# Kernel optimization log

Measured on AMD Instinct MI355X. Metric: run time of the kernel, lower is better.

The kernel has to match this reference:

```python
import jax, jax.numpy as jnp
import numpy as np

N = 4_194_304      # number of coordinate samples
H = 4              # hidden_features
L = 256            # hidden_layers
FIRST_OMEGA = 3000.0
HIDDEN_OMEGA = 30.0


def setup_inputs() -> dict:
    key = jax.random.key(0)
    ks = jax.random.split(key, 11)
    coords = jax.random.normal(ks[0], (N, 1), dtype=jnp.float32)
    # first layer: weight uniform(-1/in_features, 1/in_features), in_features=1
    w_first = jax.random.uniform(ks[1], (H, 1), jnp.float32, -1.0, 1.0)
    b_first = jax.random.uniform(ks[2], (H,), jnp.float32, -1.0, 1.0)
    # hidden layers: uniform(-sqrt(6/H)/omega, +)
    c_hid = float(np.sqrt(6.0 / H) / HIDDEN_OMEGA)
    w_hidden = jax.random.uniform(ks[3], (L, H, H), jnp.float32, -c_hid, c_hid)
    b_hidden = jax.random.uniform(ks[4], (L, H), jnp.float32, -c_hid, c_hid)
    # outermost linear, same init const
    w_out = jax.random.uniform(ks[5], (1, H), jnp.float32, -c_hid, c_hid)
    b_out = jax.random.uniform(ks[6], (1,), jnp.float32, -c_hid, c_hid)
    # harmonizer scalars (a,b,c,d); near 0 so exp(a)~1
    a_param = (jax.random.normal(ks[7], (), jnp.float32) * 0.1)
    b_param = (jax.random.normal(ks[8], (), jnp.float32) * 0.1)
    c_param = (jax.random.normal(ks[9], (), jnp.float32) * 0.1)
    d_param = (jax.random.normal(ks[10], (), jnp.float32) * 0.1)
    return {
        "coords": coords,
        "w_first": w_first, "b_first": b_first,
        "w_hidden": w_hidden, "b_hidden": b_hidden,
        "w_out": w_out, "b_out": b_out,
        "a_param": a_param, "b_param": b_param,
        "c_param": c_param, "d_param": d_param,
    }


def reference(coords, w_first, b_first, w_hidden, b_hidden, w_out, b_out,
              a_param, b_param, c_param, d_param):
    amp = jnp.exp(a_param)
    freq = jnp.exp(b_param)
    # first sine layer, omega_0 = 3000
    x = amp * jnp.sin(freq * FIRST_OMEGA * (coords @ w_first.T + b_first) + c_param) + d_param
    # 256 hidden sine layers, omega_0 = 30, via scan over the stacked weights
    def step(h, wb):
        W, bvec = wb  # W: [H,H], bvec: [H]
        h = amp * jnp.sin(freq * HIDDEN_OMEGA * (h @ W.T + bvec) + c_param) + d_param
        return h, None
    x, _ = jax.lax.scan(step, x, (w_hidden, b_hidden))
    # outermost plain linear
    return x @ w_out.T + b_out
```

## Files before the change

### kernel.cpp

```cpp
#include <hip/hip_runtime.h>
#include <math.h>

#define NSAMP 4194304
#define LAYERS 256
#define SPT 8

#define WS_W 16

__global__ void prep_kernel(
    const float* __restrict__ w_hidden, const float* __restrict__ b_hidden,
    const float* __restrict__ w_out,   const float* __restrict__ b_out,
    const float* __restrict__ a_param, const float* __restrict__ b_param,
    const float* __restrict__ c_param, const float* __restrict__ d_param,
    float* __restrict__ ws)
{
  const double TWO_PI = 6.283185307179586476925286766559;
  int idx = blockIdx.x * blockDim.x + threadIdx.x;
  float freqf = (float)exp((double)b_param[0]);
  float gf    = (float)((double)freqf * 30.0);
  float ampf  = (float)exp((double)a_param[0]);
  double scale = (double)gf / TWO_PI;
  double dd = (double)d_param[0];
  if (idx < 4096) {
    int l = idx >> 4, r = idx & 15;
    float wv = (float)((double)w_hidden[idx] * scale * (double)ampf);
    ws[WS_W + l * 20 + r] = wv;
  } else if (idx < 5120) {
    int bi = idx - 4096;
    int l = bi >> 2, i = bi & 3;
    double rs = 0.0;
    for (int j = 0; j < 4; ++j) rs += (double)w_hidden[l*16 + i*4 + j];
    double bv = ((double)gf * (double)b_hidden[bi] + (double)c_param[0]) / TWO_PI
              + dd * scale * rs;
    ws[WS_W + l * 20 + 16 + i] = (float)bv;
  } else if (idx == 5120) {
    ws[0] = (float)((double)freqf * 3000.0);
    ws[1] = c_param[0];
    double bo = (double)b_out[0]
              + dd * ((double)w_out[0] + (double)w_out[1] +
                      (double)w_out[2] + (double)w_out[3]);
    ws[2] = (float)bo;
    ws[3] = (float)((double)ampf * (double)w_out[0]);
    ws[4] = (float)((double)ampf * (double)w_out[1]);
    ws[5] = (float)((double)ampf * (double)w_out[2]);
    ws[6] = (float)((double)ampf * (double)w_out[3]);
  }
}

#if defined(__has_builtin)
#if __has_builtin(__builtin_amdgcn_sinf)
#define HAVE_SINF_BUILTIN 1
#endif
#endif

__device__ __forceinline__ float vsin_rev(float x) {
#ifdef HAVE_SINF_BUILTIN
  return __builtin_amdgcn_sinf(x);
#else
  float r;
  asm("v_sin_f32 %0, %1" : "=v"(r) : "v"(x));
  return r;
#endif
}

__device__ __forceinline__ float sin_first(float A) {
  double x = (double)A;
  double kd = rint(x * 0.31830988618379067154);
  double r  = fma(-kd, 3.1415926535897931159979634685, x);
  r = fma(-kd, 1.2246467991473531772e-16, r);
  double r2 = r * r;
  double p = 1.6059043836821613e-10;
  p = fma(r2, p, -2.5052108385441718775e-8);
  p = fma(r2, p,  2.7557319223985890653e-6);
  p = fma(r2, p, -1.9841269841269841270e-4);
  p = fma(r2, p,  8.3333333333333333333e-3);
  p = fma(r2, p, -1.6666666666666666667e-1);
  double s = fma(r2 * r, p, r);
  int ki = (int)kd;
  if (ki & 1) s = -s;
  return (float)s;
}

__global__ __launch_bounds__(256) void siren_main(
    const float* __restrict__ coords,
    const float* __restrict__ w_first, const float* __restrict__ b_first,
    const float* __restrict__ ws, float* __restrict__ out)
{
  const int tid = blockIdx.x * blockDim.x + threadIdx.x;
  const float f3000 = ws[0], cpar = ws[1];

  float c[SPT];
  const float4* cp4 = reinterpret_cast<const float4*>(coords) + tid * (SPT / 4);
#pragma unroll
  for (int q = 0; q < SPT / 4; ++q) {
    float4 v = cp4[q];
    c[4*q+0] = v.x; c[4*q+1] = v.y; c[4*q+2] = v.z; c[4*q+3] = v.w;
  }

  float wf[4], bf[4];
#pragma unroll
  for (int i = 0; i < 4; ++i) { wf[i] = w_first[i]; bf[i] = b_first[i]; }

  float sp[SPT][4];
#pragma unroll
  for (int s = 0; s < SPT; ++s) {
#pragma unroll
    for (int i = 0; i < 4; ++i) {
      float t = __fmul_rn(c[s], wf[i]);
      t = __fadd_rn(t, bf[i]);
      float A = __fadd_rn(__fmul_rn(f3000, t), cpar);
      sp[s][i] = sin_first(A);
    }
  }

  const float* __restrict__ Wb = ws + WS_W;

#define STEP(WREG)                                                      \
  {                                                                     \
    _Pragma("unroll")                                                   \
    for (int s = 0; s < SPT; ++s) {                                     \
      float z0 = fmaf(WREG[0],  sp[s][0], WREG[16]);                    \
      z0 = fmaf(WREG[1],  sp[s][1], z0);                                \
      z0 = fmaf(WREG[2],  sp[s][2], z0);                                \
      z0 = fmaf(WREG[3],  sp[s][3], z0);                                \
      float z1 = fmaf(WREG[4],  sp[s][0], WREG[17]);                    \
      z1 = fmaf(WREG[5],  sp[s][1], z1);                                \
      z1 = fmaf(WREG[6],  sp[s][2], z1);                                \
      z1 = fmaf(WREG[7],  sp[s][3], z1);                                \
      float z2 = fmaf(WREG[8],  sp[s][0], WREG[18]);                    \
      z2 = fmaf(WREG[9],  sp[s][1], z2);                                \
      z2 = fmaf(WREG[10], sp[s][2], z2);                                \
      z2 = fmaf(WREG[11], sp[s][3], z2);                                \
      float z3 = fmaf(WREG[12], sp[s][0], WREG[19]);                    \
      z3 = fmaf(WREG[13], sp[s][1], z3);                                \
      z3 = fmaf(WREG[14], sp[s][2], z3);                                \
      z3 = fmaf(WREG[15], sp[s][3], z3);                                \
      sp[s][0] = vsin_rev(z0);                                          \
      sp[s][1] = vsin_rev(z1);                                          \
      sp[s][2] = vsin_rev(z2);                                          \
      sp[s][3] = vsin_rev(z3);                                          \
    }                                                                   \
  }

  float wA[20], wB[20];
#pragma unroll
  for (int k = 0; k < 20; ++k) wA[k] = Wb[k];

  for (int l = 0; l < LAYERS; l += 2) {
    const float* p1 = Wb + (l + 1) * 20;
#pragma unroll
    for (int k = 0; k < 20; ++k) wB[k] = p1[k];
    STEP(wA);
    if (l + 2 < LAYERS) {
      const float* p2 = Wb + (l + 2) * 20;
#pragma unroll
      for (int k = 0; k < 20; ++k) wA[k] = p2[k];
    }
    STEP(wB);
  }
#undef STEP

  const float wo0 = ws[3], wo1 = ws[4], wo2 = ws[5], wo3 = ws[6], bo = ws[2];
  float o[SPT];
#pragma unroll
  for (int s = 0; s < SPT; ++s) {
    float acc = fmaf(sp[s][0], wo0, bo);
    acc = fmaf(sp[s][1], wo1, acc);
    acc = fmaf(sp[s][2], wo2, acc);
    acc = fmaf(sp[s][3], wo3, acc);
    o[s] = acc;
  }
  float4* op4 = reinterpret_cast<float4*>(out) + tid * (SPT / 4);
  float4 v0 = { o[0], o[1], o[2], o[3] };
  float4 v1 = { o[4], o[5], o[6], o[7] };
  op4[0] = v0;
  op4[1] = v1;
}

extern "C" void kernel_launch(void* const* d_in, const int* in_sizes, int n_in,
                              void* d_out, int out_size, void* d_ws, size_t ws_size,
                              hipStream_t stream) {
  const float* coords   = (const float*)d_in[0];
  const float* w_first  = (const float*)d_in[1];
  const float* b_first  = (const float*)d_in[2];
  const float* w_hidden = (const float*)d_in[3];
  const float* b_hidden = (const float*)d_in[4];
  const float* w_out    = (const float*)d_in[5];
  const float* b_out    = (const float*)d_in[6];
  const float* a_param  = (const float*)d_in[7];
  const float* b_param  = (const float*)d_in[8];
  const float* c_param  = (const float*)d_in[9];
  const float* d_param  = (const float*)d_in[10];
  float* ws   = (float*)d_ws;
  float* outp = (float*)d_out;

  prep_kernel<<<21, 256, 0, stream>>>(w_hidden, b_hidden, w_out, b_out,
                                      a_param, b_param, c_param, d_param, ws);

  const int threads = NSAMP / SPT;
  siren_main<<<threads / 256, 256, 0, stream>>>(coords, w_first, b_first, ws, outp);
}
```

Before: 723.8 us.

## Replace hardware sine with packed polynomial sine and pack hidden-layer FMAs

Hidden-layer activations are regrouped into pairs of samples held in 2-wide float vectors. Both the 4x4 matrix-vector product and a new polynomial sine are computed with packed v_pk_fma/add/mul_f32 inline assembly. The sine does range reduction in revolutions with a magic-number round, followed by an odd degree-15 polynomial. This replaces the hardware v_sin_f32 instruction with packed full-rate ALU work, and weights and biases are read as doubles so they can serve as scalar operand pairs. The trade-off is more instructions per sine, reliance on hand-written asm and on the operand modifiers being correct, and possible accuracy differences from the hardware sine.

```diff
diff --git a/kernel.cpp b/kernel.cpp
--- a/kernel.cpp
+++ b/kernel.cpp
@@ -4,6 +4,9 @@
 #define NSAMP 4194304
 #define LAYERS 256
 #define SPT 8
+#define NPAIR (SPT/2)
+
+typedef float f32x2 __attribute__((ext_vector_type(2)));
 
 #define WS_W 16
 
@@ -47,22 +50,6 @@
   }
 }
 
-#if defined(__has_builtin)
-#if __has_builtin(__builtin_amdgcn_sinf)
-#define HAVE_SINF_BUILTIN 1
-#endif
-#endif
-
-__device__ __forceinline__ float vsin_rev(float x) {
-#ifdef HAVE_SINF_BUILTIN
-  return __builtin_amdgcn_sinf(x);
-#else
-  float r;
-  asm("v_sin_f32 %0, %1" : "=v"(r) : "v"(x));
-  return r;
-#endif
-}
-
 __device__ __forceinline__ float sin_first(float A) {
   double x = (double)A;
   double kd = rint(x * 0.31830988618379067154);
@@ -81,6 +68,48 @@
   return (float)s;
 }
 
+#define PK_ADD(d, a, b) \
+  asm("v_pk_add_f32 %0, %1, %2" : "=v"(d) : "v"(a), "v"(b))
+#define PK_SUB(d, a, b) \
+  asm("v_pk_add_f32 %0, %1, %2 neg_lo:[0,1] neg_hi:[0,1]" : "=v"(d) : "v"(a), "v"(b))
+#define PK_MUL(d, a, b) \
+  asm("v_pk_mul_f32 %0, %1, %2" : "=v"(d) : "v"(a), "v"(b))
+#define PK_FMA_CS(d, a, b, cs) \
+  asm("v_pk_fma_f32 %0, %1, %2, %3 op_sel:[0,0,0] op_sel_hi:[1,1,0]" \
+      : "=v"(d) : "v"(a), "v"(b), "s"(cs))
+#define PK_FMA_WB_LO(z, w2, s, c) \
+  asm("v_pk_fma_f32 %0, %1, %2, %3 op_sel:[0,0,0] op_sel_hi:[0,1,1]" \
+      : "=v"(z) : "s"(w2), "v"(s), "v"(c))
+#define PK_FMA_WACC_LO(z, w2, s) \
+  asm("v_pk_fma_f32 %0, %1, %2, %0 op_sel:[0,0,0] op_sel_hi:[0,1,1]" \
+      : "+v"(z) : "s"(w2), "v"(s))
+#define PK_FMA_WACC_HI(z, w2, s) \
+  asm("v_pk_fma_f32 %0, %1, %2, %0 op_sel:[1,0,0] op_sel_hi:[1,1,1]" \
+      : "+v"(z) : "s"(w2), "v"(s))
+
+template <typename T, typename F>
+constexpr T bc(F f) { return __builtin_bit_cast(T, f); }
+constexpr double PKC(float f) {
+  return bc<double>((unsigned long long)bc<unsigned int>(f));
+}
+
+#define PK_SIN(dst, z, magicv, c15v, C13, C11, C9, C7, C5, C3, C1)  \
+  {                                                                 \
+    f32x2 t_, u_, r_, r2_, p_;                                      \
+    PK_ADD(t_, z, magicv);                                          \
+    PK_SUB(u_, t_, magicv);                        \
+    PK_SUB(r_, z, u_);                        \
+    PK_MUL(r2_, r_, r_);                                            \
+    PK_FMA_CS(p_, r2_, c15v, C13);                                  \
+    PK_FMA_CS(p_, p_, r2_, C11);                                    \
+    PK_FMA_CS(p_, p_, r2_, C9);                                     \
+    PK_FMA_CS(p_, p_, r2_, C7);                                     \
+    PK_FMA_CS(p_, p_, r2_, C5);                                     \
+    PK_FMA_CS(p_, p_, r2_, C3);                                     \
+    PK_FMA_CS(p_, p_, r2_, C1);                                     \
+    PK_MUL(dst, r_, p_);                                            \
+  }
+
 __global__ __launch_bounds__(256) void siren_main(
     const float* __restrict__ coords,
     const float* __restrict__ w_first, const float* __restrict__ b_first,
@@ -101,74 +130,104 @@
 #pragma unroll
   for (int i = 0; i < 4; ++i) { wf[i] = w_first[i]; bf[i] = b_first[i]; }
 
-  float sp[SPT][4];
-#pragma unroll
-  for (int s = 0; s < SPT; ++s) {
-#pragma unroll
-    for (int i = 0; i < 4; ++i) {
-      float t = __fmul_rn(c[s], wf[i]);
-      t = __fadd_rn(t, bf[i]);
-      float A = __fadd_rn(__fmul_rn(f3000, t), cpar);
-      sp[s][i] = sin_first(A);
+  f32x2 sp0[NPAIR], sp1[NPAIR], sp2[NPAIR], sp3[NPAIR];
+#pragma unroll
+  for (int p = 0; p < NPAIR; ++p) {
+    float sf[2][4];
+#pragma unroll
+    for (int h = 0; h < 2; ++h) {
+      int s = 2 * p + h;
+#pragma unroll
+      for (int i = 0; i < 4; ++i) {
+        float t = __fmul_rn(c[s], wf[i]);
+        t = __fadd_rn(t, bf[i]);
+        float A = __fadd_rn(__fmul_rn(f3000, t), cpar);
+        sf[h][i] = sin_first(A);
+      }
     }
-  }
-
-  const float* __restrict__ Wb = ws + WS_W;
-
-#define STEP(WREG)                                                      \
-  {                                                                     \
-    _Pragma("unroll")                                                   \
-    for (int s = 0; s < SPT; ++s) {                                     \
-      float z0 = fmaf(WREG[0],  sp[s][0], WREG[16]);                    \
-      z0 = fmaf(WREG[1],  sp[s][1], z0);                                \
-      z0 = fmaf(WREG[2],  sp[s][2], z0);                                \
-      z0 = fmaf(WREG[3],  sp[s][3], z0);                                \
-      float z1 = fmaf(WREG[4],  sp[s][0], WREG[17]);                    \
-      z1 = fmaf(WREG[5],  sp[s][1], z1);                                \
-      z1 = fmaf(WREG[6],  sp[s][2], z1);                                \
-      z1 = fmaf(WREG[7],  sp[s][3], z1);                                \
-      float z2 = fmaf(WREG[8],  sp[s][0], WREG[18]);                    \
-      z2 = fmaf(WREG[9],  sp[s][1], z2);                                \
-      z2 = fmaf(WREG[10], sp[s][2], z2);                                \
-      z2 = fmaf(WREG[11], sp[s][3], z2);                                \
-      float z3 = fmaf(WREG[12], sp[s][0], WREG[19]);                    \
-      z3 = fmaf(WREG[13], sp[s][1], z3);                                \
-      z3 = fmaf(WREG[14], sp[s][2], z3);                                \
-      z3 = fmaf(WREG[15], sp[s][3], z3);                                \
-      sp[s][0] = vsin_rev(z0);                                          \
-      sp[s][1] = vsin_rev(z1);                                          \
-      sp[s][2] = vsin_rev(z2);                                          \
-      sp[s][3] = vsin_rev(z3);                                          \
-    }                                                                   \
-  }
-
-  float wA[20], wB[20];
-#pragma unroll
-  for (int k = 0; k < 20; ++k) wA[k] = Wb[k];
+    f32x2 v0 = { sf[0][0], sf[1][0] }; sp0[p] = v0;
+    f32x2 v1 = { sf[0][1], sf[1][1] }; sp1[p] = v1;
+    f32x2 v2 = { sf[0][2], sf[1][2] }; sp2[p] = v2;
+    f32x2 v3 = { sf[0][3], sf[1][3] }; sp3[p] = v3;
+  }
+
+  const double C13 = PKC( 3.8199525848482823f);
+  const double C11 = PKC(-15.094642576822022f);
+  const double C9  = PKC( 42.058693944897630f);
+  const double C7  = PKC(-76.705859753061358f);
+  const double C5  = PKC( 81.605249276075034f);
+  const double C3  = PKC(-41.341702240399755f);
+  const double C1  = PKC( 6.2831853071795865f);
+  const f32x2 magicv = { 12582912.0f, 12582912.0f };
+  const f32x2 c15v   = { -0.71812927501929344f, -0.71812927501929344f };
+
+  const double* __restrict__ Wd = reinterpret_cast<const double*>(ws + WS_W);
+
+#define STEP(W0,W1,W2,W3,W4,W5,W6,W7,W8,W9)                              \
+  {                                                                      \
+    float b0_ = bc<float>((unsigned int)(bc<unsigned long long>(W8)));   \
+    float b1_ = bc<float>((unsigned int)(bc<unsigned long long>(W8)>>32));\
+    float b2_ = bc<float>((unsigned int)(bc<unsigned long long>(W9)));   \
+    float b3_ = bc<float>((unsigned int)(bc<unsigned long long>(W9)>>32));\
+    f32x2 bs0 = { b0_, b0_ }, bs1 = { b1_, b1_ };                        \
+    f32x2 bs2 = { b2_, b2_ }, bs3 = { b3_, b3_ };                        \
+    _Pragma("unroll")                                                    \
+    for (int p = 0; p < NPAIR; ++p) {                                    \
+      f32x2 z0, z1, z2, z3;                                              \
+      PK_FMA_WB_LO (z0, W0, sp0[p], bs0);                                \
+      PK_FMA_WACC_HI(z0, W0, sp1[p]);                                    \
+      PK_FMA_WACC_LO(z0, W1, sp2[p]);                                    \
+      PK_FMA_WACC_HI(z0, W1, sp3[p]);                                    \
+      PK_FMA_WB_LO (z1, W2, sp0[p], bs1);                                \
+      PK_FMA_WACC_HI(z1, W2, sp1[p]);                                    \
+      PK_FMA_WACC_LO(z1, W3, sp2[p]);                                    \
+      PK_FMA_WACC_HI(z1, W3, sp3[p]);                                    \
+      PK_FMA_WB_LO (z2, W4, sp0[p], bs2);                                \
+      PK_FMA_WACC_HI(z2, W4, sp1[p]);                                    \
+      PK_FMA_WACC_LO(z2, W5, sp2[p]);                                    \
+      PK_FMA_WACC_HI(z2, W5, sp3[p]);                                    \
+      PK_FMA_WB_LO (z3, W6, sp0[p], bs3);                                \
+      PK_FMA_WACC_HI(z3, W6, sp1[p]);                                    \
+      PK_FMA_WACC_LO(z3, W7, sp2[p]);                                    \
+      PK_FMA_WACC_HI(z3, W7, sp3[p]);                                    \
+      PK_SIN(sp0[p], z0, magicv, c15v, C13, C11, C9, C7, C5, C3, C1);    \
+      PK_SIN(sp1[p], z1, magicv, c15v, C13, C11, C9, C7, C5, C3, C1);    \
+      PK_SIN(sp2[p], z2, magicv, c15v, C13, C11, C9, C7, C5, C3, C1);    \
+      PK_SIN(sp3[p], z3, magicv, c15v, C13, C11, C9, C7, C5, C3, C1);    \
+    }                                                                    \
+  }
+
+#define LOADW(P, l)                                                      \
+  P##0 = Wd[(l)*10+0]; P##1 = Wd[(l)*10+1]; P##2 = Wd[(l)*10+2];         \
+  P##3 = Wd[(l)*10+3]; P##4 = Wd[(l)*10+4]; P##5 = Wd[(l)*10+5];         \
+  P##6 = Wd[(l)*10+6]; P##7 = Wd[(l)*10+7]; P##8 = Wd[(l)*10+8];         \
+  P##9 = Wd[(l)*10+9];
+
+  double wA0,wA1,wA2,wA3,wA4,wA5,wA6,wA7,wA8,wA9;
+  double wB0,wB1,wB2,wB3,wB4,wB5,wB6,wB7,wB8,wB9;
+  LOADW(wA, 0)
 
   for (int l = 0; l < LAYERS; l += 2) {
-    const float* p1 = Wb + (l + 1) * 20;
-#pragma unroll
-    for (int k = 0; k < 20; ++k) wB[k] = p1[k];
-    STEP(wA);
-    if (l + 2 < LAYERS) {
-      const float* p2 = Wb + (l + 2) * 20;
-#pragma unroll
-      for (int k = 0; k < 20; ++k) wA[k] = p2[k];
-    }
-    STEP(wB);
+    LOADW(wB, l + 1)
+    STEP(wA0,wA1,wA2,wA3,wA4,wA5,wA6,wA7,wA8,wA9)
+    if (l + 2 < LAYERS) { LOADW(wA, l + 2) }
+    STEP(wB0,wB1,wB2,wB3,wB4,wB5,wB6,wB7,wB8,wB9)
   }
 #undef STEP
+#undef LOADW
 
   const float wo0 = ws[3], wo1 = ws[4], wo2 = ws[5], wo3 = ws[6], bo = ws[2];
   float o[SPT];
 #pragma unroll
-  for (int s = 0; s < SPT; ++s) {
-    float acc = fmaf(sp[s][0], wo0, bo);
-    acc = fmaf(sp[s][1], wo1, acc);
-    acc = fmaf(sp[s][2], wo2, acc);
-    acc = fmaf(sp[s][3], wo3, acc);
-    o[s] = acc;
+  for (int p = 0; p < NPAIR; ++p) {
+#pragma unroll
+    for (int h = 0; h < 2; ++h) {
+      float acc = fmaf(h ? sp0[p].y : sp0[p].x, wo0, bo);
+      acc = fmaf(h ? sp1[p].y : sp1[p].x, wo1, acc);
+      acc = fmaf(h ? sp2[p].y : sp2[p].x, wo2, acc);
+      acc = fmaf(h ? sp3[p].y : sp3[p].x, wo3, acc);
+      o[2*p+h] = acc;
+    }
   }
   float4* op4 = reinterpret_cast<float4*>(out) + tid * (SPT / 4);
   float4 v0 = { o[0], o[1], o[2], o[3] };
```

Result: slower. 997.3 us (+37.8%).
